# Optimization experiments

Hardware: AMD Instinct MI355X
Metric: run time of the kernel (lower is better)

The kernel has to match this reference:

```python
import jax, jax.numpy as jnp
import numpy as np

B, S, D, F, E, TOP_K = 4, 2048, 1024, 4096, 8, 2


def setup_inputs() -> dict:
    key = jax.random.key(0)
    ks = jax.random.split(key, 6)
    sd = 1.0 / np.sqrt(D)
    sf = 1.0 / np.sqrt(F)
    return {
        "x": jax.random.normal(ks[0], (B, S, D), dtype=jnp.float32),
        "router_w": jax.random.normal(ks[1], (E, D), dtype=jnp.float32) * sd,
        "router_b": jnp.zeros((E,), dtype=jnp.float32),
        "w1": jax.random.normal(ks[2], (E, F, D), dtype=jnp.float32) * sd,  # Linear(d_model->d_ff) weight [out,in]
        "w2": jax.random.normal(ks[3], (E, D, F), dtype=jnp.float32) * sf,  # Linear(d_ff->d_model)
        "w3": jax.random.normal(ks[4], (E, F, D), dtype=jnp.float32) * sd,
    }


def reference(x, router_w, router_b, w1, w2, w3):
    # Router: softmax over experts, then top-k with renormalized gates.
    logits = jnp.einsum("bsd,ed->bse", x, router_w) + router_b          # [B,S,E]
    probs = jax.nn.softmax(logits, axis=-1)
    topk_p, topk_i = jax.lax.top_k(probs, TOP_K)                         # [B,S,K]
    topk_p = topk_p / jnp.sum(topk_p, axis=-1, keepdims=True)
    # Per-token combine weight for each expert (0 if not selected).
    combine = jnp.sum(jax.nn.one_hot(topk_i, E, dtype=x.dtype) * topk_p[..., None], axis=-2)  # [B,S,E]

    # Note: expert(x*mask)*mask == expert(x)*mask since SwiGLU(0)=0 (no bias).
    out = jnp.zeros_like(x)
    for e in range(E):  # small fixed expert count
        h = jax.nn.silu(jnp.einsum("bsd,fd->bsf", x, w1[e])) * jnp.einsum("bsd,fd->bsf", x, w3[e])
        out = out + combine[..., e:e + 1] * jnp.einsum("bsf,df->bsd", h, w2[e])
    return out
```

## Files before the change

### kernel.cpp

```cpp
#include <hip/hip_runtime.h>
#include <hip/hip_fp16.h>


#define NTOK 8192
#define D_ 1024
#define F_ 4096
#define E_ 8
#define SLOT_CAP 18432

using half8 = __attribute__((ext_vector_type(8))) _Float16;
using half4 = __attribute__((ext_vector_type(4))) _Float16;
using f32x4 = __attribute__((ext_vector_type(4))) float;

__device__ __forceinline__ void gload16(const void* g, void* l) {
  __builtin_amdgcn_global_load_lds((const __attribute__((address_space(1))) void*)g,
                                   (__attribute__((address_space(3))) void*)l, 16, 0, 0);
}

__global__ __launch_bounds__(256) void cvt_kernel(const float* __restrict__ src,
                                                  _Float16* __restrict__ dst, int n4) {
  int i = blockIdx.x * 256 + threadIdx.x;
  int stride = gridDim.x * 256;
  for (; i < n4; i += stride) {
    float4 v = ((const float4*)src)[i];
    half4 h;
    h.x = (_Float16)v.x; h.y = (_Float16)v.y; h.z = (_Float16)v.z; h.w = (_Float16)v.w;
    ((half4*)dst)[i] = h;
  }
}

__global__ __launch_bounds__(256) void cvt_w13_kernel(const float* __restrict__ w1,
                                                      const float* __restrict__ w3,
                                                      _Float16* __restrict__ w13, int n4) {
  int i = blockIdx.x * 256 + threadIdx.x;
  int stride = gridDim.x * 256;
  for (; i < n4; i += stride) {
    int d4 = i & 255;
    int row = i >> 8;
    int e = row >> 12, f = row & 4095;
    size_t vbase = ((size_t)e << 13) | ((size_t)(f >> 4) << 5) | (size_t)(f & 15);
    float4 v1 = ((const float4*)w1)[i];
    float4 v3 = ((const float4*)w3)[i];
    half4 h1, h3;
    h1.x = (_Float16)v1.x; h1.y = (_Float16)v1.y; h1.z = (_Float16)v1.z; h1.w = (_Float16)v1.w;
    h3.x = (_Float16)v3.x; h3.y = (_Float16)v3.y; h3.z = (_Float16)v3.z; h3.w = (_Float16)v3.w;
    ((half4*)w13)[vbase * 256 + d4] = h1;
    ((half4*)w13)[(vbase + 16) * 256 + d4] = h3;
  }
}

__global__ __launch_bounds__(256) void router_kernel(
    const float* __restrict__ x, const float* __restrict__ rw, const float* __restrict__ rbias,
    _Float16* __restrict__ x16, int* __restrict__ tok_e, float* __restrict__ tok_g,
    int* __restrict__ counts) {
  int wv = threadIdx.x >> 6, lane = threadIdx.x & 63;
  int t = blockIdx.x * 4 + wv;
  const float4* xr = (const float4*)(x + (size_t)t * D_);
  float acc[E_];
#pragma unroll
  for (int e = 0; e < E_; ++e) acc[e] = 0.f;
  for (int i = lane; i < D_ / 4; i += 64) {
    float4 xv = xr[i];
    half4 hx;
    hx.x = (_Float16)xv.x; hx.y = (_Float16)xv.y; hx.z = (_Float16)xv.z; hx.w = (_Float16)xv.w;
    ((half4*)(x16 + (size_t)t * D_))[i] = hx;
#pragma unroll
    for (int e = 0; e < E_; ++e) {
      float4 wv4 = ((const float4*)(rw + (size_t)e * D_))[i];
      acc[e] += xv.x * wv4.x + xv.y * wv4.y + xv.z * wv4.z + xv.w * wv4.w;
    }
  }
#pragma unroll
  for (int e = 0; e < E_; ++e) {
#pragma unroll
    for (int off = 32; off > 0; off >>= 1) acc[e] += __shfl_down(acc[e], off);
  }
  if (lane == 0) {
    float p[E_], mx = -1e30f;
#pragma unroll
    for (int e = 0; e < E_; ++e) { p[e] = acc[e] + rbias[e]; mx = fmaxf(mx, p[e]); }
#pragma unroll
    for (int e = 0; e < E_; ++e) p[e] = expf(p[e] - mx);
    int i0 = 0;
#pragma unroll
    for (int e = 1; e < E_; ++e) if (p[e] > p[i0]) i0 = e;
    int i1 = (i0 == 0) ? 1 : 0;
#pragma unroll
    for (int e = 0; e < E_; ++e) if (e != i0 && p[e] > p[i1]) i1 = e;
    float s = p[i0] + p[i1];
    tok_e[t * 2] = i0; tok_e[t * 2 + 1] = i1;
    tok_g[t * 2] = p[i0] / s; tok_g[t * 2 + 1] = p[i1] / s;
    atomicAdd(&counts[i0], 1); atomicAdd(&counts[i1], 1);
  }
}

__global__ void init_kernel(int* slot_token, int* counts, int* cursor) {
  int i = blockIdx.x * 256 + threadIdx.x;
  if (blockIdx.x == 0 && threadIdx.x < E_) { counts[threadIdx.x] = 0; cursor[threadIdx.x] = 0; }
  if (i < SLOT_CAP) slot_token[i] = 0;
}

__global__ void scan_kernel(const int* __restrict__ counts, int* __restrict__ offs) {
  if (threadIdx.x == 0) {
    int o = 0;
    for (int e = 0; e < E_; ++e) { offs[e] = o; o += ((counts[e] + 255) / 256) * 256; }
    offs[E_] = o;
  }
}

__global__ void scatter_kernel(const int* __restrict__ tok_e, const int* __restrict__ offs,
                               int* __restrict__ cursor, int* __restrict__ slot_token,
                               int* __restrict__ slot_of) {
  int i = blockIdx.x * 256 + threadIdx.x;
  if (i >= NTOK * 2) return;
  int e = tok_e[i];
  int pos = offs[e] + atomicAdd(&cursor[e], 1);
  slot_token[pos] = i >> 1;
  slot_of[i] = pos;
}

template <int MODE, int ORD, int KD, int NBN, int RPX, int BEROWS>
__global__ __launch_bounds__(512, 2) void moe_gemm_kernel(
    const _Float16* __restrict__ Amat, const _Float16* __restrict__ Bmat,
    const int* __restrict__ slot_token, const int* __restrict__ offs,
    void* __restrict__ outp) {
  constexpr int BM = 256;
  constexpr int MROW = 8;
  constexpr int AH = BM * 32;
  constexpr int BUFH = (BM + 256) * 32;
  constexpr int NT = KD / 32;
  __shared__ _Float16 lds[4 * BUFH];

  int id = blockIdx.x;
  int xcd = id & 7, idx = id >> 3;
  int rb, nb;
  if constexpr (ORD == 0) {
    int band = idx / (8 * NBN);
    int i2 = idx - band * (8 * NBN);
    int rib = (RPX - band * 8) < 8 ? (RPX - band * 8) : 8;
    nb = i2 / rib;
    rb = xcd * RPX + band * 8 + (i2 - nb * rib);
  } else {
    nb = idx % NBN;
    rb = xcd * RPX + idx / NBN;
  }
  int row0 = rb * BM;
  if (row0 >= offs[E_]) return;
  int e = 0;
#pragma unroll
  for (int i = 1; i < E_; ++i) if (row0 >= offs[i]) e = i;

  int t = threadIdx.x, l = t & 63, w = t >> 6;
  int wr = w >> 2, wc = w & 3;
  int srow = t >> 2;
  int gsrc8 = ((l & 3) ^ ((l >> 3) & 3)) * 8;

  const _Float16* aP0;
  const _Float16* aP1;
  if constexpr (MODE == 0) {
    int tk0 = slot_token[row0 + srow];
    int tk1 = slot_token[row0 + srow + 128];
    aP0 = Amat + (size_t)tk0 * KD + gsrc8;
    aP1 = Amat + (size_t)tk1 * KD + gsrc8;
  } else {
    aP0 = Amat + (size_t)(row0 + srow) * KD + gsrc8;
    aP1 = Amat + (size_t)(row0 + srow + 128) * KD + gsrc8;
  }
  const _Float16* b0P = Bmat + ((size_t)e * BEROWS + (size_t)nb * 256 + srow) * KD + gsrc8;
  const _Float16* b1P = b0P + (size_t)128 * KD;

  int fr = l & 15, kg = l >> 4;
  int swz8 = (kg ^ ((fr >> 1) & 3)) * 8;
  const int rA = (wr * 128 + fr) * 32 + swz8;
  const int rB = AH + (wc * 64 + fr) * 32 + swz8;

  half8 aF[MROW];
  half8 bF[4];
  f32x4 acc[MROW][4];
#pragma unroll
  for (int m = 0; m < MROW; ++m)
#pragma unroll
    for (int n = 0; n < 4; ++n) acc[m][n] = (f32x4){0.f, 0.f, 0.f, 0.f};

#pragma unroll
  for (int tt = 0; tt < 3; ++tt) {
    gload16(aP0 + tt * 32, &lds[tt * BUFH + w * 512]);
    gload16(aP1 + tt * 32, &lds[tt * BUFH + 4096 + w * 512]);
    gload16(b0P + tt * 32, &lds[tt * BUFH + AH + w * 512]);
    gload16(b1P + tt * 32, &lds[tt * BUFH + AH + 4096 + w * 512]);
  }
  asm volatile("s_waitcnt vmcnt(4)" ::: "memory");
  __builtin_amdgcn_s_barrier();
  __builtin_amdgcn_sched_barrier(0);
#pragma unroll
  for (int m = 0; m < MROW; ++m) aF[m] = *(const half8*)&lds[rA + m * 512];
#pragma unroll
  for (int n = 0; n < 4; ++n) bF[n] = *(const half8*)&lds[rB + n * 512];
  __builtin_amdgcn_sched_barrier(0);
  aP0 += 96; aP1 += 96; b0P += 96; b1P += 96;

#define MF4_(mm)                                                                         \
  acc[mm][0] = __builtin_amdgcn_mfma_f32_16x16x32_f16(aF[mm], bF[0], acc[mm][0], 0, 0, 0); \
  acc[mm][1] = __builtin_amdgcn_mfma_f32_16x16x32_f16(aF[mm], bF[1], acc[mm][1], 0, 0, 0); \
  acc[mm][2] = __builtin_amdgcn_mfma_f32_16x16x32_f16(aF[mm], bF[2], acc[mm][2], 0, 0, 0); \
  acc[mm][3] = __builtin_amdgcn_mfma_f32_16x16x32_f16(aF[mm], bF[3], acc[mm][3], 0, 0, 0);

#define GSTEP(U, PRE, WN)                                                     \
  {                                                                           \
    constexpr int bn_ = ((U) + 1) & 3;                                        \
    constexpr int bs_ = ((U) + 3) & 3;                                        \
    if (PRE) {                                                                \
      gload16(aP0 + (U) * 32, &lds[bs_ * BUFH + w * 512]);                    \
      gload16(aP1 + (U) * 32, &lds[bs_ * BUFH + 4096 + w * 512]);             \
      gload16(b0P + (U) * 32, &lds[bs_ * BUFH + AH + w * 512]);               \
      gload16(b1P + (U) * 32, &lds[bs_ * BUFH + AH + 4096 + w * 512]);        \
    }                                                                         \
    const _Float16* nb_ = &lds[bn_ * BUFH];                                   \
    asm volatile("s_waitcnt lgkmcnt(0)" ::: "memory");                        \
    __builtin_amdgcn_sched_barrier(0);                                        \
    __builtin_amdgcn_s_setprio(1);                                            \
    MF4_(0) aF[0] = *(const half8*)(nb_ + rA);                                \
    MF4_(1) aF[1] = *(const half8*)(nb_ + rA + 512);                          \
    MF4_(2) aF[2] = *(const half8*)(nb_ + rA + 1024);                         \
    MF4_(3) aF[3] = *(const half8*)(nb_ + rA + 1536);                         \
    MF4_(4) aF[4] = *(const half8*)(nb_ + rA + 2048);                         \
    MF4_(5) aF[5] = *(const half8*)(nb_ + rA + 2560);                         \
    MF4_(6) aF[6] = *(const half8*)(nb_ + rA + 3072);                         \
    MF4_(7) aF[7] = *(const half8*)(nb_ + rA + 3584);                         \
    bF[0] = *(const half8*)(nb_ + rB);                                        \
    bF[1] = *(const half8*)(nb_ + rB + 512);                                  \
    bF[2] = *(const half8*)(nb_ + rB + 1024);                                 \
    bF[3] = *(const half8*)(nb_ + rB + 1536);                                 \
    __builtin_amdgcn_s_setprio(0);                                            \
    if ((WN) >= 0) {                                                          \
      asm volatile("s_waitcnt vmcnt(%0)" ::"i"((WN) >= 0 ? (WN) : 0) : "memory"); \
      __builtin_amdgcn_s_barrier();                                           \
      __builtin_amdgcn_sched_barrier(0);                                      \
    }                                                                         \
  }

  for (int j4 = 0; j4 < NT - 4; j4 += 4) {
    GSTEP(0, true, 4)
    GSTEP(1, true, 4)
    GSTEP(2, true, 4)
    GSTEP(3, true, 4)
    aP0 += 128; aP1 += 128; b0P += 128; b1P += 128;
  }
  GSTEP(0, true, 4)
  GSTEP(1, false, 0)
  GSTEP(2, false, -1)
  asm volatile("s_waitcnt lgkmcnt(0)" ::: "memory");
  __builtin_amdgcn_sched_barrier(0);
  __builtin_amdgcn_s_setprio(1);
  MF4_(0) MF4_(1) MF4_(2) MF4_(3) MF4_(4) MF4_(5) MF4_(6) MF4_(7)
  __builtin_amdgcn_s_setprio(0);
#undef GSTEP
#undef MF4_

  int q4 = kg * 4;
  if constexpr (MODE == 0) {
    _Float16* hb = (_Float16*)outp;
#pragma unroll
    for (int mi = 0; mi < MROW; ++mi) {
      size_t rbase = (size_t)(row0 + wr * 128 + mi * 16 + q4);
#pragma unroll
      for (int p = 0; p < 2; ++p) {
        int fc = nb * 128 + (wc * 2 + p) * 16 + fr;
#pragma unroll
        for (int i = 0; i < 4; ++i) {
          float gv = acc[mi][2 * p][i];
          float hv = gv / (1.f + __expf(-gv)) * acc[mi][2 * p + 1][i];
          hb[(rbase + i) * (size_t)F_ + fc] = (_Float16)hv;
        }
      }
    }
  } else {
    float* yb = (float*)outp;
#pragma unroll
    for (int mi = 0; mi < MROW; ++mi) {
      size_t rbase = (size_t)(row0 + wr * 128 + mi * 16 + q4);
#pragma unroll
      for (int ni = 0; ni < 4; ++ni) {
        int col = nb * 256 + wc * 64 + ni * 16 + fr;
#pragma unroll
        for (int i = 0; i < 4; ++i)
          yb[(rbase + i) * (size_t)D_ + col] = acc[mi][ni][i];
      }
    }
  }
}

__global__ __launch_bounds__(256) void combine_kernel(
    const float* __restrict__ ybuf, const int* __restrict__ slot_of,
    const float* __restrict__ tok_g, float* __restrict__ out) {
  int t = blockIdx.x, i = threadIdx.x;
  int s0 = slot_of[t * 2], s1 = slot_of[t * 2 + 1];
  float g0 = tok_g[t * 2], g1 = tok_g[t * 2 + 1];
  float4 a = ((const float4*)(ybuf + (size_t)s0 * D_))[i];
  float4 b = ((const float4*)(ybuf + (size_t)s1 * D_))[i];
  float4 r;
  r.x = g0 * a.x + g1 * b.x;
  r.y = g0 * a.y + g1 * b.y;
  r.z = g0 * a.z + g1 * b.z;
  r.w = g0 * a.w + g1 * b.w;
  ((float4*)(out + (size_t)t * D_))[i] = r;
}

extern "C" void kernel_launch(void* const* d_in, const int* in_sizes, int n_in,
                              void* d_out, int out_size, void* d_ws, size_t ws_size,
                              hipStream_t stream) {
  const float* x  = (const float*)d_in[0];
  const float* rw = (const float*)d_in[1];
  const float* rbc = (const float*)d_in[2];
  const float* w1 = (const float*)d_in[3];
  const float* w2 = (const float*)d_in[4];
  const float* w3 = (const float*)d_in[5];
  float* out = (float*)d_out;

  char* ws = (char*)d_ws;
  size_t off = 0;
  auto take = [&](size_t bytes) {
    char* p = ws + off;
    off = (off + bytes + 255) & ~(size_t)255;
    return p;
  };
  _Float16* x16 = (_Float16*)take((size_t)NTOK * D_ * 2);
  _Float16* w13 = (_Float16*)take((size_t)E_ * 2 * F_ * D_ * 2);
  _Float16* w2h = (_Float16*)take((size_t)E_ * D_ * F_ * 2);
  _Float16* hbuf = (_Float16*)take((size_t)SLOT_CAP * F_ * 2);
  float* ybuf = (float*)take((size_t)SLOT_CAP * D_ * 4);
  int* slot_token = (int*)take((size_t)SLOT_CAP * 4);
  int* tok_e = (int*)take((size_t)NTOK * 2 * 4);
  float* tok_g = (float*)take((size_t)NTOK * 2 * 4);
  int* slot_of = (int*)take((size_t)NTOK * 2 * 4);
  int* counts = (int*)take(E_ * 4);
  int* cursor = (int*)take(E_ * 4);
  int* offs = (int*)take((E_ + 1) * 4);

  cvt_w13_kernel<<<4096, 256, 0, stream>>>(w1, w3, w13, E_ * F_ * D_ / 4);
  cvt_kernel<<<4096, 256, 0, stream>>>(w2, w2h, E_ * D_ * F_ / 4);
  init_kernel<<<(SLOT_CAP + 255) / 256, 256, 0, stream>>>(slot_token, counts, cursor);
  router_kernel<<<NTOK / 4, 256, 0, stream>>>(x, rw, rbc, x16, tok_e, tok_g, counts);
  scan_kernel<<<1, 64, 0, stream>>>(counts, offs);
  scatter_kernel<<<(NTOK * 2 + 255) / 256, 256, 0, stream>>>(tok_e, offs, cursor, slot_token, slot_of);
  moe_gemm_kernel<0, 0, 1024, 32, 9, 8192><<<2304, 512, 0, stream>>>(
      x16, w13, slot_token, offs, (void*)hbuf);
  moe_gemm_kernel<1, 1, 4096, 4, 9, 1024><<<288, 512, 0, stream>>>(
      hbuf, w2h, slot_token, offs, (void*)ybuf);
  combine_kernel<<<NTOK, 256, 0, stream>>>(ybuf, slot_of, tok_g, out);
}
```

Baseline: 912.5 us.

## Split-K the down-projection GEMM and double-buffer B fragments with sched group barriers

```diff
diff --git a/kernel.cpp b/kernel.cpp
--- a/kernel.cpp
+++ b/kernel.cpp
@@ -119,36 +119,40 @@
   slot_of[i] = pos;
 }
 
-template <int MODE, int ORD, int KD, int NBN, int RPX, int BEROWS>
+template <int MODE, int ORD, int KSPLIT, int KD, int NBN, int RPX, int BEROWS>
 __global__ __launch_bounds__(512, 2) void moe_gemm_kernel(
     const _Float16* __restrict__ Amat, const _Float16* __restrict__ Bmat,
     const int* __restrict__ slot_token, const int* __restrict__ offs,
-    void* __restrict__ outp) {
+    void* __restrict__ outp, void* __restrict__ outp2) {
   constexpr int BM = 256;
   constexpr int MROW = 8;
   constexpr int AH = BM * 32;
   constexpr int BUFH = (BM + 256) * 32;
-  constexpr int NT = KD / 32;
+  constexpr int KL = KD / KSPLIT;
+  constexpr int NT = KL / 32;
   __shared__ _Float16 lds[4 * BUFH];
 
   int id = blockIdx.x;
   int xcd = id & 7, idx = id >> 3;
-  int rb, nb;
+  int vr, nb;
   if constexpr (ORD == 0) {
     int band = idx / (8 * NBN);
     int i2 = idx - band * (8 * NBN);
     int rib = (RPX - band * 8) < 8 ? (RPX - band * 8) : 8;
     nb = i2 / rib;
-    rb = xcd * RPX + band * 8 + (i2 - nb * rib);
+    vr = xcd * RPX + band * 8 + (i2 - nb * rib);
   } else {
     nb = idx % NBN;
-    rb = xcd * RPX + idx / NBN;
-  }
+    vr = xcd * RPX + idx / NBN;
+  }
+  int rb = vr, ks = 0;
+  if constexpr (KSPLIT == 2) { rb = vr >> 1; ks = vr & 1; }
   int row0 = rb * BM;
   if (row0 >= offs[E_]) return;
   int e = 0;
 #pragma unroll
   for (int i = 1; i < E_; ++i) if (row0 >= offs[i]) e = i;
+  int koff = ks * KL;
 
   int t = threadIdx.x, l = t & 63, w = t >> 6;
   int wr = w >> 2, wc = w & 3;
@@ -160,13 +164,14 @@
   if constexpr (MODE == 0) {
     int tk0 = slot_token[row0 + srow];
     int tk1 = slot_token[row0 + srow + 128];
-    aP0 = Amat + (size_t)tk0 * KD + gsrc8;
-    aP1 = Amat + (size_t)tk1 * KD + gsrc8;
+    aP0 = Amat + (size_t)tk0 * KD + koff + gsrc8;
+    aP1 = Amat + (size_t)tk1 * KD + koff + gsrc8;
   } else {
-    aP0 = Amat + (size_t)(row0 + srow) * KD + gsrc8;
-    aP1 = Amat + (size_t)(row0 + srow + 128) * KD + gsrc8;
-  }
-  const _Float16* b0P = Bmat + ((size_t)e * BEROWS + (size_t)nb * 256 + srow) * KD + gsrc8;
+    aP0 = Amat + (size_t)(row0 + srow) * KD + koff + gsrc8;
+    aP1 = Amat + (size_t)(row0 + srow + 128) * KD + koff + gsrc8;
+  }
+  const _Float16* b0P =
+      Bmat + ((size_t)e * BEROWS + (size_t)nb * 256 + srow) * KD + koff + gsrc8;
   const _Float16* b1P = b0P + (size_t)128 * KD;
 
   int fr = l & 15, kg = l >> 4;
@@ -175,7 +180,7 @@
   const int rB = AH + (wc * 64 + fr) * 32 + swz8;
 
   half8 aF[MROW];
-  half8 bF[4];
+  half8 bF[4], bF2[4];
   f32x4 acc[MROW][4];
 #pragma unroll
   for (int m = 0; m < MROW; ++m)
@@ -199,63 +204,72 @@
   __builtin_amdgcn_sched_barrier(0);
   aP0 += 96; aP1 += 96; b0P += 96; b1P += 96;
 
-#define MF4_(mm)                                                                         \
-  acc[mm][0] = __builtin_amdgcn_mfma_f32_16x16x32_f16(aF[mm], bF[0], acc[mm][0], 0, 0, 0); \
-  acc[mm][1] = __builtin_amdgcn_mfma_f32_16x16x32_f16(aF[mm], bF[1], acc[mm][1], 0, 0, 0); \
-  acc[mm][2] = __builtin_amdgcn_mfma_f32_16x16x32_f16(aF[mm], bF[2], acc[mm][2], 0, 0, 0); \
-  acc[mm][3] = __builtin_amdgcn_mfma_f32_16x16x32_f16(aF[mm], bF[3], acc[mm][3], 0, 0, 0);
-
-#define GSTEP(U, PRE, WN)                                                     \
-  {                                                                           \
-    constexpr int bn_ = ((U) + 1) & 3;                                        \
-    constexpr int bs_ = ((U) + 3) & 3;                                        \
-    if (PRE) {                                                                \
-      gload16(aP0 + (U) * 32, &lds[bs_ * BUFH + w * 512]);                    \
-      gload16(aP1 + (U) * 32, &lds[bs_ * BUFH + 4096 + w * 512]);             \
-      gload16(b0P + (U) * 32, &lds[bs_ * BUFH + AH + w * 512]);               \
-      gload16(b1P + (U) * 32, &lds[bs_ * BUFH + AH + 4096 + w * 512]);        \
-    }                                                                         \
-    const _Float16* nb_ = &lds[bn_ * BUFH];                                   \
-    asm volatile("s_waitcnt lgkmcnt(0)" ::: "memory");                        \
-    __builtin_amdgcn_sched_barrier(0);                                        \
-    __builtin_amdgcn_s_setprio(1);                                            \
-    MF4_(0) aF[0] = *(const half8*)(nb_ + rA);                                \
-    MF4_(1) aF[1] = *(const half8*)(nb_ + rA + 512);                          \
-    MF4_(2) aF[2] = *(const half8*)(nb_ + rA + 1024);                         \
-    MF4_(3) aF[3] = *(const half8*)(nb_ + rA + 1536);                         \
-    MF4_(4) aF[4] = *(const half8*)(nb_ + rA + 2048);                         \
-    MF4_(5) aF[5] = *(const half8*)(nb_ + rA + 2560);                         \
-    MF4_(6) aF[6] = *(const half8*)(nb_ + rA + 3072);                         \
-    MF4_(7) aF[7] = *(const half8*)(nb_ + rA + 3584);                         \
-    bF[0] = *(const half8*)(nb_ + rB);                                        \
-    bF[1] = *(const half8*)(nb_ + rB + 512);                                  \
-    bF[2] = *(const half8*)(nb_ + rB + 1024);                                 \
-    bF[3] = *(const half8*)(nb_ + rB + 1536);                                 \
-    __builtin_amdgcn_s_setprio(0);                                            \
-    if ((WN) >= 0) {                                                          \
+#define SGB_(m, n) __builtin_amdgcn_sched_group_barrier(m, n, 0)
+#define MF4B(mm, BU)                                                                       \
+  acc[mm][0] = __builtin_amdgcn_mfma_f32_16x16x32_f16(aF[mm], BU[0], acc[mm][0], 0, 0, 0); \
+  acc[mm][1] = __builtin_amdgcn_mfma_f32_16x16x32_f16(aF[mm], BU[1], acc[mm][1], 0, 0, 0); \
+  acc[mm][2] = __builtin_amdgcn_mfma_f32_16x16x32_f16(aF[mm], BU[2], acc[mm][2], 0, 0, 0); \
+  acc[mm][3] = __builtin_amdgcn_mfma_f32_16x16x32_f16(aF[mm], BU[3], acc[mm][3], 0, 0, 0);
+
+#define GSTEP(U, PRE, WN, BU, BR)                                                 \
+  {                                                                               \
+    constexpr int bn_ = ((U) + 1) & 3;                                            \
+    constexpr int bs_ = ((U) + 3) & 3;                                            \
+    __builtin_amdgcn_s_setprio(1);                                                \
+    if (PRE) {                                                                    \
+      gload16(aP0 + (U) * 32, &lds[bs_ * BUFH + w * 512]);                        \
+      gload16(aP1 + (U) * 32, &lds[bs_ * BUFH + 4096 + w * 512]);                 \
+      gload16(b0P + (U) * 32, &lds[bs_ * BUFH + AH + w * 512]);                   \
+      gload16(b1P + (U) * 32, &lds[bs_ * BUFH + AH + 4096 + w * 512]);            \
+    }                                                                             \
+    const _Float16* nb_ = &lds[bn_ * BUFH];                                       \
+    BR[0] = *(const half8*)(nb_ + rB);                                            \
+    BR[1] = *(const half8*)(nb_ + rB + 512);                                      \
+    BR[2] = *(const half8*)(nb_ + rB + 1024);                                     \
+    BR[3] = *(const half8*)(nb_ + rB + 1536);                                     \
+    MF4B(0, BU) aF[0] = *(const half8*)(nb_ + rA);                                \
+    MF4B(1, BU) aF[1] = *(const half8*)(nb_ + rA + 512);                          \
+    MF4B(2, BU) aF[2] = *(const half8*)(nb_ + rA + 1024);                         \
+    MF4B(3, BU) aF[3] = *(const half8*)(nb_ + rA + 1536);                         \
+    MF4B(4, BU) aF[4] = *(const half8*)(nb_ + rA + 2048);                         \
+    MF4B(5, BU) aF[5] = *(const half8*)(nb_ + rA + 2560);                         \
+    MF4B(6, BU) aF[6] = *(const half8*)(nb_ + rA + 3072);                         \
+    MF4B(7, BU) aF[7] = *(const half8*)(nb_ + rA + 3584);                         \
+    if (PRE) SGB_(0x20, 4);                                                       \
+    SGB_(0x100, 4);                                                               \
+    SGB_(0x8, 4); SGB_(0x100, 1);                                                 \
+    SGB_(0x8, 4); SGB_(0x100, 1);                                                 \
+    SGB_(0x8, 4); SGB_(0x100, 1);                                                 \
+    SGB_(0x8, 4); SGB_(0x100, 1);                                                 \
+    SGB_(0x8, 4); SGB_(0x100, 1);                                                 \
+    SGB_(0x8, 4); SGB_(0x100, 1);                                                 \
+    SGB_(0x8, 4); SGB_(0x100, 1);                                                 \
+    SGB_(0x8, 4); SGB_(0x100, 1);                                                 \
+    __builtin_amdgcn_s_setprio(0);                                                \
+    if ((WN) >= 0) {                                                              \
       asm volatile("s_waitcnt vmcnt(%0)" ::"i"((WN) >= 0 ? (WN) : 0) : "memory"); \
-      __builtin_amdgcn_s_barrier();                                           \
-      __builtin_amdgcn_sched_barrier(0);                                      \
-    }                                                                         \
+      __builtin_amdgcn_s_barrier();                                               \
+      __builtin_amdgcn_sched_barrier(0);                                          \
+    }                                                                             \
   }
 
   for (int j4 = 0; j4 < NT - 4; j4 += 4) {
-    GSTEP(0, true, 4)
-    GSTEP(1, true, 4)
-    GSTEP(2, true, 4)
-    GSTEP(3, true, 4)
+    GSTEP(0, true, 4, bF, bF2)
+    GSTEP(1, true, 4, bF2, bF)
+    GSTEP(2, true, 4, bF, bF2)
+    GSTEP(3, true, 4, bF2, bF)
     aP0 += 128; aP1 += 128; b0P += 128; b1P += 128;
   }
-  GSTEP(0, true, 4)
-  GSTEP(1, false, 0)
-  GSTEP(2, false, -1)
-  asm volatile("s_waitcnt lgkmcnt(0)" ::: "memory");
-  __builtin_amdgcn_sched_barrier(0);
+  GSTEP(0, true, 4, bF, bF2)
+  GSTEP(1, false, 0, bF2, bF)
+  GSTEP(2, false, -1, bF, bF2)
   __builtin_amdgcn_s_setprio(1);
-  MF4_(0) MF4_(1) MF4_(2) MF4_(3) MF4_(4) MF4_(5) MF4_(6) MF4_(7)
+  MF4B(0, bF2) MF4B(1, bF2) MF4B(2, bF2) MF4B(3, bF2)
+  MF4B(4, bF2) MF4B(5, bF2) MF4B(6, bF2) MF4B(7, bF2)
   __builtin_amdgcn_s_setprio(0);
 #undef GSTEP
-#undef MF4_
+#undef MF4B
+#undef SGB_
 
   int q4 = kg * 4;
   if constexpr (MODE == 0) {
@@ -275,7 +289,7 @@
       }
     }
   } else {
-    float* yb = (float*)outp;
+    float* yb = (float*)(ks == 0 ? outp : outp2);
 #pragma unroll
     for (int mi = 0; mi < MROW; ++mi) {
       size_t rbase = (size_t)(row0 + wr * 128 + mi * 16 + q4);
@@ -291,18 +305,21 @@
 }
 
 __global__ __launch_bounds__(256) void combine_kernel(
-    const float* __restrict__ ybuf, const int* __restrict__ slot_of,
-    const float* __restrict__ tok_g, float* __restrict__ out) {
+    const float* __restrict__ ya, const float* __restrict__ yb2,
+    const int* __restrict__ slot_of, const float* __restrict__ tok_g,
+    float* __restrict__ out) {
   int t = blockIdx.x, i = threadIdx.x;
   int s0 = slot_of[t * 2], s1 = slot_of[t * 2 + 1];
   float g0 = tok_g[t * 2], g1 = tok_g[t * 2 + 1];
-  float4 a = ((const float4*)(ybuf + (size_t)s0 * D_))[i];
-  float4 b = ((const float4*)(ybuf + (size_t)s1 * D_))[i];
+  float4 a0 = ((const float4*)(ya + (size_t)s0 * D_))[i];
+  float4 a1 = ((const float4*)(yb2 + (size_t)s0 * D_))[i];
+  float4 b0 = ((const float4*)(ya + (size_t)s1 * D_))[i];
+  float4 b1 = ((const float4*)(yb2 + (size_t)s1 * D_))[i];
   float4 r;
-  r.x = g0 * a.x + g1 * b.x;
-  r.y = g0 * a.y + g1 * b.y;
-  r.z = g0 * a.z + g1 * b.z;
-  r.w = g0 * a.w + g1 * b.w;
+  r.x = g0 * (a0.x + a1.x) + g1 * (b0.x + b1.x);
+  r.y = g0 * (a0.y + a1.y) + g1 * (b0.y + b1.y);
+  r.z = g0 * (a0.z + a1.z) + g1 * (b0.z + b1.z);
+  r.w = g0 * (a0.w + a1.w) + g1 * (b0.w + b1.w);
   ((float4*)(out + (size_t)t * D_))[i] = r;
 }
 
@@ -336,6 +353,7 @@
   int* counts = (int*)take(E_ * 4);
   int* cursor = (int*)take(E_ * 4);
   int* offs = (int*)take((E_ + 1) * 4);
+  float* ybuf2 = (float*)w13;
 
   cvt_w13_kernel<<<4096, 256, 0, stream>>>(w1, w3, w13, E_ * F_ * D_ / 4);
   cvt_kernel<<<4096, 256, 0, stream>>>(w2, w2h, E_ * D_ * F_ / 4);
@@ -343,9 +361,9 @@
   router_kernel<<<NTOK / 4, 256, 0, stream>>>(x, rw, rbc, x16, tok_e, tok_g, counts);
   scan_kernel<<<1, 64, 0, stream>>>(counts, offs);
   scatter_kernel<<<(NTOK * 2 + 255) / 256, 256, 0, stream>>>(tok_e, offs, cursor, slot_token, slot_of);
-  moe_gemm_kernel<0, 0, 1024, 32, 9, 8192><<<2304, 512, 0, stream>>>(
-      x16, w13, slot_token, offs, (void*)hbuf);
-  moe_gemm_kernel<1, 1, 4096, 4, 9, 1024><<<288, 512, 0, stream>>>(
-      hbuf, w2h, slot_token, offs, (void*)ybuf);
-  combine_kernel<<<NTOK, 256, 0, stream>>>(ybuf, slot_of, tok_g, out);
-}
+  moe_gemm_kernel<0, 0, 1, 1024, 32, 9, 8192><<<2304, 512, 0, stream>>>(
+      x16, w13, slot_token, offs, (void*)hbuf, nullptr);
+  moe_gemm_kernel<1, 1, 2, 4096, 4, 18, 1024><<<576, 512, 0, stream>>>(
+      hbuf, w2h, slot_token, offs, (void*)ybuf, (void*)ybuf2);
+  combine_kernel<<<NTOK, 256, 0, stream>>>(ybuf, ybuf2, slot_of, tok_g, out);
+}
```

Measured after the change: 900.7 us. About the same (-1.3%).
